# Optimization experiments

Measured on AMD Instinct MI355X. Metric: run time of the kernel, lower is better.

## Reference

```python
import jax, jax.numpy as jnp
import numpy as np


def setup_inputs() -> dict:
    key = jax.random.key(0)
    k1, k2 = jax.random.split(key)
    B, D, T = 8, 256, 4096
    Q, K = 8, 1024
    z = jax.random.normal(k1, (B, D, T), dtype=jnp.float32)
    # original init: uniform(-1/n_e, 1/n_e)
    codebooks = jax.random.uniform(k2, (Q, K, D), dtype=jnp.float32,
                                   minval=-1.0 / K, maxval=1.0 / K)
    return {"z": z, "codebooks": codebooks}


def reference(z, codebooks):
    # z: [B, e_dim, T]; codebooks: [Q, n_e, e_dim]
    zp = jnp.transpose(z, (0, 2, 1))  # [B, T, D]
    residual = zp
    quantized_out = jnp.zeros_like(zp)
    total_loss = jnp.zeros((), dtype=z.dtype)
    all_indices = []
    Q = codebooks.shape[0]
    for q in range(Q):  # small fixed number of residual stages
        E = codebooks[q]  # [K, D]
        # squared euclidean distances: ||r||^2 + ||e||^2 - 2 r.e
        d = (jnp.sum(residual ** 2, axis=-1, keepdims=True)
             + jnp.sum(E ** 2, axis=-1)
             - 2.0 * jnp.einsum('btd,kd->btk', residual, E))  # [B, T, K]
        idx = jnp.argmin(d, axis=-1)  # [B, T]
        z_q = E[idx]                  # [B, T, D] gather
        loss = (jnp.mean((jax.lax.stop_gradient(z_q) - residual) ** 2)
                + 0.25 * jnp.mean((z_q - jax.lax.stop_gradient(residual)) ** 2))
        # straight-through estimator
        z_q_st = residual + jax.lax.stop_gradient(z_q - residual)
        residual = residual - z_q_st
        quantized_out = quantized_out + z_q_st
        total_loss = total_loss + loss
        all_indices.append(idx)
    quantized_out = jnp.transpose(quantized_out, (0, 2, 1))  # [B, D, T]
    return quantized_out, total_loss, jnp.stack(all_indices)  # indices: [Q, B, T]
```

## Files before the change

kernel.cpp:

```cpp
#include <hip/hip_runtime.h>

#define B_   8
#define D_   256
#define T_   4096
#define Q_   8
#define K_   1024
#define BT_  (B_*T_)
#define N_   (B_*T_*D_)
#define LOSS_OFF N_
#define IDX_OFF  (N_+1)
#define ROWS 32

typedef __attribute__((ext_vector_type(8))) short short8;
typedef __attribute__((ext_vector_type(4))) float float4v;

union U4S8 { uint4 u; short8 s; };

__device__ __forceinline__ unsigned short f2bf(float x) {
    unsigned int u = __float_as_uint(x);
    unsigned int r = (u + 0x7FFFu + ((u >> 16) & 1u)) >> 16;
    return (unsigned short)r;
}
__device__ __forceinline__ float bf2f(unsigned short b) {
    return __uint_as_float(((unsigned int)b) << 16);
}
__device__ __forceinline__ unsigned fkey(float f) {
    unsigned u = __float_as_uint(f);
    return (u & 0x80000000u) ? ~u : (u | 0x80000000u);
}
__device__ __forceinline__ float fkeyinv(unsigned k) {
    unsigned u = (k & 0x80000000u) ? (k & 0x7fffffffu) : ~k;
    return __uint_as_float(u);
}


__global__ void k_init(const float* __restrict__ z, float* __restrict__ residual,
                       double* lossAcc, unsigned* MelU) {
    __shared__ float tile[32][33];
    int b  = blockIdx.z;
    int d0 = blockIdx.y * 32;
    int t0 = blockIdx.x * 32;
    int tx = threadIdx.x & 31;
    int ty = threadIdx.x >> 5;
    const float* zb = z + (size_t)b * D_ * T_;
    #pragma unroll
    for (int r = 0; r < 32; r += 8)
        tile[ty + r][tx] = zb[(size_t)(d0 + ty + r) * T_ + t0 + tx];
    __syncthreads();
    float* rb = residual + (size_t)b * T_ * D_;
    #pragma unroll
    for (int r = 0; r < 32; r += 8)
        rb[(size_t)(t0 + ty + r) * D_ + d0 + tx] = tile[tx][ty + r];
    if (b == 0 && blockIdx.x == 0 && blockIdx.y == 0 && threadIdx.x == 0) {
        *lossAcc = 0.0;
        #pragma unroll
        for (int i = 0; i < Q_; ++i) MelU[i] = 0u;
    }
}


__global__ void k_bfrag(const float* __restrict__ cb, uint4* __restrict__ Bfrag) {
    int gid = blockIdx.x * 256 + threadIdx.x;
    int q    = gid >> 15;
    int rem  = gid & 32767;
    int ct   = rem >> 9;
    int kc   = (rem >> 6) & 7;
    int lane = rem & 63;
    int cand = ct * 16 + (lane & 15);
    int kb   = kc * 32 + (lane >> 4) * 8;
    const float* e = cb + ((size_t)q * K_ + cand) * D_ + kb;
    float4v u0 = *(const float4v*)(e);
    float4v u1 = *(const float4v*)(e + 4);
    float vv[8] = {u0.x, u0.y, u0.z, u0.w, u1.x, u1.y, u1.z, u1.w};
    unsigned short h[8], l[8];
    #pragma unroll
    for (int j = 0; j < 8; ++j) {
        float v = vv[j];
        h[j] = f2bf(v);
        l[j] = f2bf(v - bf2f(h[j]));
    }
    uint4 hi, lo;
    hi.x = (unsigned)h[0] | ((unsigned)h[1] << 16);
    hi.y = (unsigned)h[2] | ((unsigned)h[3] << 16);
    hi.z = (unsigned)h[4] | ((unsigned)h[5] << 16);
    hi.w = (unsigned)h[6] | ((unsigned)h[7] << 16);
    lo.x = (unsigned)l[0] | ((unsigned)l[1] << 16);
    lo.y = (unsigned)l[2] | ((unsigned)l[3] << 16);
    lo.z = (unsigned)l[4] | ((unsigned)l[5] << 16);
    lo.w = (unsigned)l[6] | ((unsigned)l[7] << 16);
    size_t base = (((size_t)(q * 64 + ct) * 8 + kc) * 2) * 64;
    Bfrag[base + lane]      = hi;
    Bfrag[base + 64 + lane] = lo;
}


__global__ void k_se(const float* __restrict__ cb, float* __restrict__ Se,
                     unsigned* __restrict__ MelU) {
    int gid = blockIdx.x * 256 + threadIdx.x;
    int i  = gid >> 4;
    int ln = gid & 15;
    if (i >= Q_ * K_) return;
    const float* e = cb + (size_t)i * D_ + ln * 16;
    float4v v0 = *(const float4v*)(e);
    float4v v1 = *(const float4v*)(e + 4);
    float4v v2 = *(const float4v*)(e + 8);
    float4v v3 = *(const float4v*)(e + 12);
    float vv[16] = {v0.x, v0.y, v0.z, v0.w, v1.x, v1.y, v1.z, v1.w,
                    v2.x, v2.y, v2.z, v2.w, v3.x, v3.y, v3.z, v3.w};
    double s = 0.0, s2 = 0.0;
    #pragma unroll
    for (int d = 0; d < 16; ++d) {
        float v = vv[d];
        float a = v * v;
        s += (double)a;
        float el = v - bf2f(f2bf(v));
        s2 += (double)(el * el);
    }
    #pragma unroll
    for (int st = 8; st > 0; st >>= 1) {
        s  += __shfl_xor(s, st);
        s2 += __shfl_xor(s2, st);
    }
    if (ln == 0) {
        Se[i] = (float)s;
        atomicMax(&MelU[i >> 10], __float_as_uint((float)s2));
    }
}


__launch_bounds__(512, 2)
__global__ void k_stage(const float* __restrict__ cb,
                        const uint4* __restrict__ Bfrag,
                        const float* __restrict__ Se,
                        const float* __restrict__ Mel,
                        float* __restrict__ residual,
                        float* __restrict__ out,
                        double* __restrict__ lossAcc,
                        int q) {
    __shared__ union {
        uint4 afr[2048];
        struct { int slist[32][16]; float sdd[32][16];
                 int srow[512]; int sslot[512]; } post;
        struct { float ovd[512]; int ovk[512]; } over;
        double lred[8];
    } sc;
    __shared__ float seL[1024];
    __shared__ float srb[32], margin[32];
    __shared__ unsigned sminI[32];
    __shared__ int   scount[32], sidx[32];
    __shared__ int   nSurv;

    const int tid  = threadIdx.x;
    const int lane = tid & 63;
    const int w    = tid >> 6;
    const int quad = lane >> 4;
    const int lc   = lane & 15;
    const int row0 = blockIdx.x * ROWS;
    const int g    = tid >> 8;
    const int dt   = tid & 255;

    if (tid < 32) { scount[tid] = 0; sminI[tid] = 0xFFFFFFFFu; }
    if (tid == 32) nSurv = 0;
    seL[tid]       = Se[q * K_ + tid];
    seL[tid + 512] = Se[q * K_ + tid + 512];
    const float melq4 = 4.04f * sqrtf(Mel[q]);

    const uint4* __restrict__ Bq = Bfrag + (size_t)q * (64 * 8 * 2 * 64);
    U4S8 b0h, b1h;
    {
        const uint4* p0 = Bq + (((size_t)((w * 8 + 0) * 8 + 0)) * 2) * 64 + lane;
        b0h.u = p0[0];
        const uint4* p1 = Bq + (((size_t)((w * 8 + 1) * 8 + 0)) * 2) * 64 + lane;
        b1h.u = p1[0];
    }

    {
        int row = tid >> 4, seg = tid & 15;
        int rg = row >> 4, rlo = row & 15;
        int kc = seg >> 1, par = seg & 1;
        const float* rp = residual + (size_t)(row0 + row) * D_ + seg * 16;
        float4v v0 = *(const float4v*)(rp);
        float4v v1 = *(const float4v*)(rp + 4);
        float4v v2 = *(const float4v*)(rp + 8);
        float4v v3 = *(const float4v*)(rp + 12);
        float vv[16] = {v0.x, v0.y, v0.z, v0.w, v1.x, v1.y, v1.z, v1.w,
                        v2.x, v2.y, v2.z, v2.w, v3.x, v3.y, v3.z, v3.w};
        double s = 0.0; float sa = 0.0f;
        #pragma unroll
        for (int i = 0; i < 16; ++i) {
            float v = vv[i];
            s += (double)(v * v);
            sa += fabsf(v);
        }
        #pragma unroll
        for (int st = 8; st > 0; st >>= 1) {
            s  += __shfl_xor(s, st);
            sa += __shfl_xor(sa, st);
        }
        if (seg == 0) {
            float sr = (float)s;
            float sb = sa * 1.001f;
            srb[row]    = sr;
            margin[row] = 9.6e-7f * sr + 4.0e-7f * sb + 2.0e-4f
                        + melq4 * sqrtf(sr);
        }
        #pragma unroll
        for (int h = 0; h < 2; ++h) {
            unsigned short hh[8], ll[8];
            #pragma unroll
            for (int j = 0; j < 8; ++j) {
                float v = vv[h * 8 + j];
                hh[j] = f2bf(v);
                ll[j] = f2bf(v - bf2f(hh[j]));
            }
            uint4 hiW, loW;
            hiW.x = (unsigned)hh[0] | ((unsigned)hh[1] << 16);
            hiW.y = (unsigned)hh[2] | ((unsigned)hh[3] << 16);
            hiW.z = (unsigned)hh[4] | ((unsigned)hh[5] << 16);
            hiW.w = (unsigned)hh[6] | ((unsigned)hh[7] << 16);
            loW.x = (unsigned)ll[0] | ((unsigned)ll[1] << 16);
            loW.y = (unsigned)ll[2] | ((unsigned)ll[3] << 16);
            loW.z = (unsigned)ll[4] | ((unsigned)ll[5] << 16);
            loW.w = (unsigned)ll[6] | ((unsigned)ll[7] << 16);
            int ln = (par * 2 + h) * 16 + rlo;
            int sl = ln ^ kc;
            sc.afr[((rg * 8 + kc) * 2 + 0) * 64 + sl] = hiW;
            sc.afr[((rg * 8 + kc) * 2 + 1) * 64 + sl] = loW;
        }
    }
    __syncthreads();

    float4v accA[16];
    #pragma unroll
    for (int i = 0; i < 16; ++i) accA[i] = (float4v){0.f, 0.f, 0.f, 0.f};

    for (int kc = 0; kc < 8; ++kc) {
        U4S8 a0h, a0l, a1h, a1l;
        a0h.u = sc.afr[((0 * 8 + kc) * 2 + 0) * 64 + (lane ^ kc)];
        a0l.u = sc.afr[((0 * 8 + kc) * 2 + 1) * 64 + (lane ^ kc)];
        a1h.u = sc.afr[((1 * 8 + kc) * 2 + 0) * 64 + (lane ^ kc)];
        a1l.u = sc.afr[((1 * 8 + kc) * 2 + 1) * 64 + (lane ^ kc)];
        #pragma unroll
        for (int ctl = 0; ctl < 8; ++ctl) {
            U4S8 bh = ((ctl & 1) == 0) ? b0h : b1h;
            {
                int pkc  = kc + ((ctl + 2) >> 3);
                int pctl = (ctl + 2) & 7;
                const uint4* p = Bq + (((size_t)((w * 8 + pctl) * 8 + pkc)) * 2) * 64 + lane;
                if ((ctl & 1) == 0) b0h.u = p[0];
                else                b1h.u = p[0];
            }
            float4v a0 = accA[ctl * 2 + 0];
            a0 = __builtin_amdgcn_mfma_f32_16x16x32_bf16(a0h.s, bh.s, a0, 0, 0, 0);
            a0 = __builtin_amdgcn_mfma_f32_16x16x32_bf16(a0l.s, bh.s, a0, 0, 0, 0);
            accA[ctl * 2 + 0] = a0;
            float4v a1 = accA[ctl * 2 + 1];
            a1 = __builtin_amdgcn_mfma_f32_16x16x32_bf16(a1h.s, bh.s, a1, 0, 0, 0);
            a1 = __builtin_amdgcn_mfma_f32_16x16x32_bf16(a1l.s, bh.s, a1, 0, 0, 0);
            accA[ctl * 2 + 1] = a1;
        }
    }

    float sr8[8];
    #pragma unroll
    for (int rr = 0; rr < 8; ++rr)
        sr8[rr] = srb[(rr >> 2) * 16 + quad * 4 + (rr & 3)];

    float mn[8];
    #pragma unroll
    for (int rr = 0; rr < 8; ++rr) mn[rr] = 3.4e38f;
    #pragma unroll
    for (int ctl = 0; ctl < 8; ++ctl) {
        int cand = (w * 8 + ctl) * 16 + lc;
        float se = seL[cand];
        #pragma unroll
        for (int rr = 0; rr < 8; ++rr) {
            float dd = (sr8[rr] + se) - 2.0f * accA[ctl * 2 + (rr >> 2)][rr & 3];
            mn[rr] = fminf(mn[rr], dd);
        }
    }
    #pragma unroll
    for (int rr = 0; rr < 8; ++rr) {
        float v = mn[rr];
        v = fminf(v, __shfl_xor(v, 1));
        v = fminf(v, __shfl_xor(v, 2));
        v = fminf(v, __shfl_xor(v, 4));
        v = fminf(v, __shfl_xor(v, 8));
        if (lc == 0)
            atomicMin(&sminI[(rr >> 2) * 16 + quad * 4 + (rr & 3)], fkey(v));
    }
    __syncthreads();

    float thrV[8];
    #pragma unroll
    for (int rr = 0; rr < 8; ++rr) {
        int row = (rr >> 2) * 16 + quad * 4 + (rr & 3);
        thrV[rr] = fkeyinv(sminI[row]) + margin[row];
    }
    #pragma unroll
    for (int ctl = 0; ctl < 8; ++ctl) {
        int cand = (w * 8 + ctl) * 16 + lc;
        float se = seL[cand];
        #pragma unroll
        for (int rr = 0; rr < 8; ++rr) {
            int row = (rr >> 2) * 16 + quad * 4 + (rr & 3);
            float dd = (sr8[rr] + se) - 2.0f * accA[ctl * 2 + (rr >> 2)][rr & 3];
            if (dd <= thrV[rr]) {
                int p = atomicAdd(&scount[row], 1);
                if (p < 16) sc.post.slist[row][p] = cand;
            }
        }
    }
    __syncthreads();

    if (tid < 32) {
        int cnt = scount[tid];
        if (cnt == 1) {
            sidx[tid] = sc.post.slist[tid][0];
        } else if (cnt >= 2 && cnt <= 16) {
            int base = atomicAdd(&nSurv, cnt);
            for (int s2 = 0; s2 < cnt; ++s2) {
                sc.post.srow[base + s2]  = tid;
                sc.post.sslot[base + s2] = s2;
            }
        }
    }
    __syncthreads();

    {
        int nS  = nSurv;
        int grp = tid >> 4, ln = tid & 15;
        for (int j = grp; j < nS; j += 32) {
            int row  = sc.post.srow[j];
            int slot = sc.post.sslot[j];
            int k    = sc.post.slist[row][slot];
            const float* Ek = cb + ((size_t)q * K_ + k) * D_ + ln * 16;
            const float* Rk = residual + (size_t)(row0 + row) * D_ + ln * 16;
            float4v e0 = *(const float4v*)(Ek);
            float4v e1 = *(const float4v*)(Ek + 4);
            float4v e2 = *(const float4v*)(Ek + 8);
            float4v e3 = *(const float4v*)(Ek + 12);
            float4v r0 = *(const float4v*)(Rk);
            float4v r1 = *(const float4v*)(Rk + 4);
            float4v r2 = *(const float4v*)(Rk + 8);
            float4v r3 = *(const float4v*)(Rk + 12);
            float ev[16] = {e0.x, e0.y, e0.z, e0.w, e1.x, e1.y, e1.z, e1.w,
                            e2.x, e2.y, e2.z, e2.w, e3.x, e3.y, e3.z, e3.w};
            float rv2[16] = {r0.x, r0.y, r0.z, r0.w, r1.x, r1.y, r1.z, r1.w,
                             r2.x, r2.y, r2.z, r2.w, r3.x, r3.y, r3.z, r3.w};
            double a0 = 0.0, a1 = 0.0;
            #pragma unroll
            for (int d = 0; d < 16; d += 2) {
                a0 = fma((double)ev[d],     (double)rv2[d],     a0);
                a1 = fma((double)ev[d + 1], (double)rv2[d + 1], a1);
            }
            double ssum = a0 + a1;
            #pragma unroll
            for (int st = 8; st > 0; st >>= 1) ssum += __shfl_xor(ssum, st);
            if (ln == 0) {
                float dotf = (float)ssum;
                float V = srb[row] + seL[k];
                sc.post.sdd[row][slot] = V - 2.0f * dotf;
            }
        }
    }
    __syncthreads();
    if (tid < 32) {
        int cnt = scount[tid];
        if (cnt >= 2 && cnt <= 16) {
            float bd = 3.4e38f; int bk = 0x7fffffff;
            for (int s2 = 0; s2 < cnt; ++s2) {
                float dv = sc.post.sdd[tid][s2]; int kv = sc.post.slist[tid][s2];
                if (dv < bd || (dv == bd && kv < bk)) { bd = dv; bk = kv; }
            }
            sidx[tid] = bk;
        }
    }
    __syncthreads();

    for (int row = 0; row < ROWS; ++row) {
        int cnt = scount[row];
        if (cnt <= 16) continue;
        const float* Rr = residual + (size_t)(row0 + row) * D_;
        float bd = 3.4e38f; int bk = K_;
        #pragma unroll
        for (int c = 0; c < 2; ++c) {
            int k = tid * 2 + c;
            const float* Ek = cb + ((size_t)q * K_ + k) * D_;
            double a0 = 0.0, a1 = 0.0;
            for (int d = 0; d < D_; d += 2) {
                a0 = fma((double)Ek[d],     (double)Rr[d],     a0);
                a1 = fma((double)Ek[d + 1], (double)Rr[d + 1], a1);
            }
            float dd = (srb[row] + seL[k]) - 2.0f * (float)(a0 + a1);
            if (dd < bd || (dd == bd && k < bk)) { bd = dd; bk = k; }
        }
        sc.over.ovd[tid] = bd; sc.over.ovk[tid] = bk;
        __syncthreads();
        for (int st = 256; st > 0; st >>= 1) {
            if (tid < st) {
                float od = sc.over.ovd[tid + st]; int ok = sc.over.ovk[tid + st];
                if (od < sc.over.ovd[tid] ||
                    (od == sc.over.ovd[tid] && ok < sc.over.ovk[tid])) {
                    sc.over.ovd[tid] = od; sc.over.ovk[tid] = ok;
                }
            }
            __syncthreads();
        }
        if (tid == 0) sidx[row] = sc.over.ovk[0];
        __syncthreads();
    }

    const float* Eq = cb + (size_t)q * K_ * D_;
    double lsum = 0.0;
    #pragma unroll
    for (int jj = 0; jj < 16; ++jj) {
        int row = g * 16 + jj;
        int idx = sidx[row];
        size_t roff = (size_t)(row0 + row) * D_ + dt;
        float rv   = residual[roff];
        float zq   = Eq[(size_t)idx * D_ + dt];
        float t1   = zq - rv;
        float zqst = rv + t1;
        residual[roff] = rv - zqst;
        lsum += (double)t1 * (double)t1;
    }
    if (tid < 32) out[IDX_OFF + q * BT_ + row0 + tid] = (float)sidx[tid];

    #pragma unroll
    for (int st = 32; st > 0; st >>= 1) lsum += __shfl_xor(lsum, st);
    __syncthreads();
    if (lane == 0) sc.lred[w] = lsum;
    __syncthreads();
    if (tid == 0) {
        double t = 0.0;
        #pragma unroll
        for (int i = 0; i < 8; ++i) t += sc.lred[i];
        atomicAdd(lossAcc, t);
    }
}


__global__ void k_emit(const float* __restrict__ z, const float* __restrict__ residual,
                       float* __restrict__ out) {
    __shared__ float tile[32][33];
    int b  = blockIdx.z;
    int t0 = blockIdx.y * 32;
    int d0 = blockIdx.x * 32;
    int tx = threadIdx.x & 31;
    int ty = threadIdx.x >> 5;
    const float* rb = residual + (size_t)b * T_ * D_;
    #pragma unroll
    for (int r = 0; r < 32; r += 8)
        tile[ty + r][tx] = rb[(size_t)(t0 + ty + r) * D_ + d0 + tx];
    __syncthreads();
    const float* zb = z + (size_t)b * D_ * T_;
    float* ob = out + (size_t)b * D_ * T_;
    #pragma unroll
    for (int r = 0; r < 32; r += 8) {
        size_t off = (size_t)(d0 + ty + r) * T_ + t0 + tx;
        ob[off] = zb[off] - tile[tx][ty + r];
    }
}

__global__ void k_final(const double* lossAcc, float* out) {
    if (threadIdx.x == 0 && blockIdx.x == 0) {
        double m = *lossAcc / (double)N_;
        out[LOSS_OFF] = (float)(1.25 * m);
    }
}


extern "C" void kernel_launch(void* const* d_in, const int* in_sizes, int n_in,
                              void* d_out, int out_size, void* d_ws, size_t ws_size,
                              hipStream_t stream) {
    const float* z  = (const float*)d_in[0];
    const float* cb = (const float*)d_in[1];
    float* out = (float*)d_out;

    float*  residual = (float*)d_ws;
    uint4*  Bfrag    = (uint4*)((char*)d_ws + (size_t)N_ * 4);
    float*  Se       = (float*)((char*)d_ws + (size_t)N_ * 4 + (size_t)8 * 1024 * 1024);
    double* lossAcc  = (double*)((char*)d_ws + (size_t)N_ * 4 + (size_t)8 * 1024 * 1024
                                 + (size_t)Q_ * K_ * 4);
    unsigned* MelU   = (unsigned*)((char*)lossAcc + 8);

    hipLaunchKernelGGL(k_init, dim3(T_ / 32, D_ / 32, B_), dim3(256), 0, stream,
                       z, residual, lossAcc, MelU);
    hipLaunchKernelGGL(k_bfrag, dim3(1024), dim3(256), 0, stream, cb, Bfrag);
    hipLaunchKernelGGL(k_se, dim3((Q_ * K_ * 16 + 255) / 256), dim3(256), 0, stream,
                       cb, Se, MelU);
    for (int q = 0; q < Q_; ++q) {
        hipLaunchKernelGGL(k_stage, dim3(BT_ / ROWS), dim3(512), 0, stream,
                           cb, Bfrag, Se, (const float*)MelU, residual, out, lossAcc, q);
    }
    hipLaunchKernelGGL(k_emit, dim3(D_ / 32, T_ / 32, B_), dim3(256), 0, stream,
                       z, residual, out);
    hipLaunchKernelGGL(k_final, dim3(1), dim3(256), 0, stream, lossAcc, out);
}
```

Baseline: 915.6 us.

## Fuse pairs of residual quantization stages into one kernel with LDS-resident residual

Each launch now processes two consecutive codebook stages for the same 32 rows. The residual tile stays in a 32KB shared buffer between the two stages and is written to global memory only after the second stage. This halves the number of stage launches and removes one global read and write of the residual per pair. The extra shared memory may lower occupancy below the two blocks per CU the launch bounds request.

```diff
diff --git a/kernel.cpp b/kernel.cpp
--- a/kernel.cpp
+++ b/kernel.cpp
@@ -129,14 +129,15 @@
 
 
 __launch_bounds__(512, 2)
-__global__ void k_stage(const float* __restrict__ cb,
-                        const uint4* __restrict__ Bfrag,
-                        const float* __restrict__ Se,
-                        const float* __restrict__ Mel,
-                        float* __restrict__ residual,
-                        float* __restrict__ out,
-                        double* __restrict__ lossAcc,
-                        int q) {
+__global__ void k_stagepair(const float* __restrict__ cb,
+                            const uint4* __restrict__ Bfrag,
+                            const float* __restrict__ Se,
+                            const float* __restrict__ Mel,
+                            float* __restrict__ residual,
+                            float* __restrict__ out,
+                            double* __restrict__ lossAcc,
+                            int q0) {
+    __shared__ float rbuf[ROWS][256];
     __shared__ union {
         uint4 afr[2048];
         struct { int slist[32][16]; float sdd[32][16];
@@ -159,277 +160,298 @@
     const int g    = tid >> 8;
     const int dt   = tid & 255;
 
-    if (tid < 32) { scount[tid] = 0; sminI[tid] = 0xFFFFFFFFu; }
-    if (tid == 32) nSurv = 0;
-    seL[tid]       = Se[q * K_ + tid];
-    seL[tid + 512] = Se[q * K_ + tid + 512];
-    const float melq4 = 4.04f * sqrtf(Mel[q]);
-
-    const uint4* __restrict__ Bq = Bfrag + (size_t)q * (64 * 8 * 2 * 64);
-    U4S8 b0h, b1h;
-    {
-        const uint4* p0 = Bq + (((size_t)((w * 8 + 0) * 8 + 0)) * 2) * 64 + lane;
-        b0h.u = p0[0];
-        const uint4* p1 = Bq + (((size_t)((w * 8 + 1) * 8 + 0)) * 2) * 64 + lane;
-        b1h.u = p1[0];
-    }
-
-    {
-        int row = tid >> 4, seg = tid & 15;
-        int rg = row >> 4, rlo = row & 15;
-        int kc = seg >> 1, par = seg & 1;
-        const float* rp = residual + (size_t)(row0 + row) * D_ + seg * 16;
-        float4v v0 = *(const float4v*)(rp);
-        float4v v1 = *(const float4v*)(rp + 4);
-        float4v v2 = *(const float4v*)(rp + 8);
-        float4v v3 = *(const float4v*)(rp + 12);
-        float vv[16] = {v0.x, v0.y, v0.z, v0.w, v1.x, v1.y, v1.z, v1.w,
-                        v2.x, v2.y, v2.z, v2.w, v3.x, v3.y, v3.z, v3.w};
-        double s = 0.0; float sa = 0.0f;
-        #pragma unroll
-        for (int i = 0; i < 16; ++i) {
-            float v = vv[i];
-            s += (double)(v * v);
-            sa += fabsf(v);
-        }
-        #pragma unroll
-        for (int st = 8; st > 0; st >>= 1) {
-            s  += __shfl_xor(s, st);
-            sa += __shfl_xor(sa, st);
-        }
-        if (seg == 0) {
-            float sr = (float)s;
-            float sb = sa * 1.001f;
-            srb[row]    = sr;
-            margin[row] = 9.6e-7f * sr + 4.0e-7f * sb + 2.0e-4f
-                        + melq4 * sqrtf(sr);
-        }
-        #pragma unroll
-        for (int h = 0; h < 2; ++h) {
-            unsigned short hh[8], ll[8];
-            #pragma unroll
-            for (int j = 0; j < 8; ++j) {
-                float v = vv[h * 8 + j];
-                hh[j] = f2bf(v);
-                ll[j] = f2bf(v - bf2f(hh[j]));
-            }
-            uint4 hiW, loW;
-            hiW.x = (unsigned)hh[0] | ((unsigned)hh[1] << 16);
-            hiW.y = (unsigned)hh[2] | ((unsigned)hh[3] << 16);
-            hiW.z = (unsigned)hh[4] | ((unsigned)hh[5] << 16);
-            hiW.w = (unsigned)hh[6] | ((unsigned)hh[7] << 16);
-            loW.x = (unsigned)ll[0] | ((unsigned)ll[1] << 16);
-            loW.y = (unsigned)ll[2] | ((unsigned)ll[3] << 16);
-            loW.z = (unsigned)ll[4] | ((unsigned)ll[5] << 16);
-            loW.w = (unsigned)ll[6] | ((unsigned)ll[7] << 16);
-            int ln = (par * 2 + h) * 16 + rlo;
-            int sl = ln ^ kc;
-            sc.afr[((rg * 8 + kc) * 2 + 0) * 64 + sl] = hiW;
-            sc.afr[((rg * 8 + kc) * 2 + 1) * 64 + sl] = loW;
-        }
-    }
-    __syncthreads();
-
-    float4v accA[16];
-    #pragma unroll
-    for (int i = 0; i < 16; ++i) accA[i] = (float4v){0.f, 0.f, 0.f, 0.f};
-
-    for (int kc = 0; kc < 8; ++kc) {
-        U4S8 a0h, a0l, a1h, a1l;
-        a0h.u = sc.afr[((0 * 8 + kc) * 2 + 0) * 64 + (lane ^ kc)];
-        a0l.u = sc.afr[((0 * 8 + kc) * 2 + 1) * 64 + (lane ^ kc)];
-        a1h.u = sc.afr[((1 * 8 + kc) * 2 + 0) * 64 + (lane ^ kc)];
-        a1l.u = sc.afr[((1 * 8 + kc) * 2 + 1) * 64 + (lane ^ kc)];
+    double lsum = 0.0;
+
+    for (int qs = 0; qs < 2; ++qs) {
+        const int q = q0 + qs;
+
+        if (tid < 32) { scount[tid] = 0; sminI[tid] = 0xFFFFFFFFu; }
+        if (tid == 32) nSurv = 0;
+        seL[tid]       = Se[q * K_ + tid];
+        seL[tid + 512] = Se[q * K_ + tid + 512];
+        const float melq4 = 4.04f * sqrtf(Mel[q]);
+
+        const uint4* __restrict__ Bq = Bfrag + (size_t)q * (64 * 8 * 2 * 64);
+        U4S8 b0h, b1h;
+        {
+            const uint4* p0 = Bq + (((size_t)((w * 8 + 0) * 8 + 0)) * 2) * 64 + lane;
+            b0h.u = p0[0];
+            const uint4* p1 = Bq + (((size_t)((w * 8 + 1) * 8 + 0)) * 2) * 64 + lane;
+            b1h.u = p1[0];
+        }
+
+        {
+            int row = tid >> 4, seg = tid & 15;
+            int rg = row >> 4, rlo = row & 15;
+            int kc = seg >> 1, par = seg & 1;
+            float4v v0, v1, v2, v3;
+            if (qs == 0) {
+                const float* rp = residual + (size_t)(row0 + row) * D_ + seg * 16;
+                v0 = *(const float4v*)(rp);
+                v1 = *(const float4v*)(rp + 4);
+                v2 = *(const float4v*)(rp + 8);
+                v3 = *(const float4v*)(rp + 12);
+                float* lp = &rbuf[row][seg * 16];
+                *(float4v*)(lp)      = v0;
+                *(float4v*)(lp + 4)  = v1;
+                *(float4v*)(lp + 8)  = v2;
+                *(float4v*)(lp + 12) = v3;
+            } else {
+                const float* lp = &rbuf[row][seg * 16];
+                v0 = *(const float4v*)(lp);
+                v1 = *(const float4v*)(lp + 4);
+                v2 = *(const float4v*)(lp + 8);
+                v3 = *(const float4v*)(lp + 12);
+            }
+            float vv[16] = {v0.x, v0.y, v0.z, v0.w, v1.x, v1.y, v1.z, v1.w,
+                            v2.x, v2.y, v2.z, v2.w, v3.x, v3.y, v3.z, v3.w};
+            double s = 0.0; float sa = 0.0f;
+            #pragma unroll
+            for (int i = 0; i < 16; ++i) {
+                float v = vv[i];
+                s += (double)(v * v);
+                sa += fabsf(v);
+            }
+            #pragma unroll
+            for (int st = 8; st > 0; st >>= 1) {
+                s  += __shfl_xor(s, st);
+                sa += __shfl_xor(sa, st);
+            }
+            if (seg == 0) {
+                float sr = (float)s;
+                float sb = sa * 1.001f;
+                srb[row]    = sr;
+                margin[row] = 9.6e-7f * sr + 4.0e-7f * sb + 2.0e-4f
+                            + melq4 * sqrtf(sr);
+            }
+            #pragma unroll
+            for (int h = 0; h < 2; ++h) {
+                unsigned short hh[8], ll[8];
+                #pragma unroll
+                for (int j = 0; j < 8; ++j) {
+                    float v = vv[h * 8 + j];
+                    hh[j] = f2bf(v);
+                    ll[j] = f2bf(v - bf2f(hh[j]));
+                }
+                uint4 hiW, loW;
+                hiW.x = (unsigned)hh[0] | ((unsigned)hh[1] << 16);
+                hiW.y = (unsigned)hh[2] | ((unsigned)hh[3] << 16);
+                hiW.z = (unsigned)hh[4] | ((unsigned)hh[5] << 16);
+                hiW.w = (unsigned)hh[6] | ((unsigned)hh[7] << 16);
+                loW.x = (unsigned)ll[0] | ((unsigned)ll[1] << 16);
+                loW.y = (unsigned)ll[2] | ((unsigned)ll[3] << 16);
+                loW.z = (unsigned)ll[4] | ((unsigned)ll[5] << 16);
+                loW.w = (unsigned)ll[6] | ((unsigned)ll[7] << 16);
+                int ln = (par * 2 + h) * 16 + rlo;
+                int sl = ln ^ kc;
+                sc.afr[((rg * 8 + kc) * 2 + 0) * 64 + sl] = hiW;
+                sc.afr[((rg * 8 + kc) * 2 + 1) * 64 + sl] = loW;
+            }
+        }
+        __syncthreads();
+
+        float4v accA[16];
+        #pragma unroll
+        for (int i = 0; i < 16; ++i) accA[i] = (float4v){0.f, 0.f, 0.f, 0.f};
+
+        for (int kc = 0; kc < 8; ++kc) {
+            U4S8 a0h, a0l, a1h, a1l;
+            a0h.u = sc.afr[((0 * 8 + kc) * 2 + 0) * 64 + (lane ^ kc)];
+            a0l.u = sc.afr[((0 * 8 + kc) * 2 + 1) * 64 + (lane ^ kc)];
+            a1h.u = sc.afr[((1 * 8 + kc) * 2 + 0) * 64 + (lane ^ kc)];
+            a1l.u = sc.afr[((1 * 8 + kc) * 2 + 1) * 64 + (lane ^ kc)];
+            #pragma unroll
+            for (int ctl = 0; ctl < 8; ++ctl) {
+                U4S8 bh = ((ctl & 1) == 0) ? b0h : b1h;
+                {
+                    int pkc  = kc + ((ctl + 2) >> 3);
+                    int pctl = (ctl + 2) & 7;
+                    const uint4* p = Bq + (((size_t)((w * 8 + pctl) * 8 + pkc)) * 2) * 64 + lane;
+                    if ((ctl & 1) == 0) b0h.u = p[0];
+                    else                b1h.u = p[0];
+                }
+                float4v a0 = accA[ctl * 2 + 0];
+                a0 = __builtin_amdgcn_mfma_f32_16x16x32_bf16(a0h.s, bh.s, a0, 0, 0, 0);
+                a0 = __builtin_amdgcn_mfma_f32_16x16x32_bf16(a0l.s, bh.s, a0, 0, 0, 0);
+                accA[ctl * 2 + 0] = a0;
+                float4v a1 = accA[ctl * 2 + 1];
+                a1 = __builtin_amdgcn_mfma_f32_16x16x32_bf16(a1h.s, bh.s, a1, 0, 0, 0);
+                a1 = __builtin_amdgcn_mfma_f32_16x16x32_bf16(a1l.s, bh.s, a1, 0, 0, 0);
+                accA[ctl * 2 + 1] = a1;
+            }
+        }
+
+        float sr8[8];
+        #pragma unroll
+        for (int rr = 0; rr < 8; ++rr)
+            sr8[rr] = srb[(rr >> 2) * 16 + quad * 4 + (rr & 3)];
+
+        float mn[8];
+        #pragma unroll
+        for (int rr = 0; rr < 8; ++rr) mn[rr] = 3.4e38f;
         #pragma unroll
         for (int ctl = 0; ctl < 8; ++ctl) {
-            U4S8 bh = ((ctl & 1) == 0) ? b0h : b1h;
-            {
-                int pkc  = kc + ((ctl + 2) >> 3);
-                int pctl = (ctl + 2) & 7;
-                const uint4* p = Bq + (((size_t)((w * 8 + pctl) * 8 + pkc)) * 2) * 64 + lane;
-                if ((ctl & 1) == 0) b0h.u = p[0];
-                else                b1h.u = p[0];
-            }
-            float4v a0 = accA[ctl * 2 + 0];
-            a0 = __builtin_amdgcn_mfma_f32_16x16x32_bf16(a0h.s, bh.s, a0, 0, 0, 0);
-            a0 = __builtin_amdgcn_mfma_f32_16x16x32_bf16(a0l.s, bh.s, a0, 0, 0, 0);
-            accA[ctl * 2 + 0] = a0;
-            float4v a1 = accA[ctl * 2 + 1];
-            a1 = __builtin_amdgcn_mfma_f32_16x16x32_bf16(a1h.s, bh.s, a1, 0, 0, 0);
-            a1 = __builtin_amdgcn_mfma_f32_16x16x32_bf16(a1l.s, bh.s, a1, 0, 0, 0);
-            accA[ctl * 2 + 1] = a1;
-        }
-    }
-
-    float sr8[8];
-    #pragma unroll
-    for (int rr = 0; rr < 8; ++rr)
-        sr8[rr] = srb[(rr >> 2) * 16 + quad * 4 + (rr & 3)];
-
-    float mn[8];
-    #pragma unroll
-    for (int rr = 0; rr < 8; ++rr) mn[rr] = 3.4e38f;
-    #pragma unroll
-    for (int ctl = 0; ctl < 8; ++ctl) {
-        int cand = (w * 8 + ctl) * 16 + lc;
-        float se = seL[cand];
+            int cand = (w * 8 + ctl) * 16 + lc;
+            float se = seL[cand];
+            #pragma unroll
+            for (int rr = 0; rr < 8; ++rr) {
+                float dd = (sr8[rr] + se) - 2.0f * accA[ctl * 2 + (rr >> 2)][rr & 3];
+                mn[rr] = fminf(mn[rr], dd);
+            }
+        }
         #pragma unroll
         for (int rr = 0; rr < 8; ++rr) {
-            float dd = (sr8[rr] + se) - 2.0f * accA[ctl * 2 + (rr >> 2)][rr & 3];
-            mn[rr] = fminf(mn[rr], dd);
-        }
-    }
-    #pragma unroll
-    for (int rr = 0; rr < 8; ++rr) {
-        float v = mn[rr];
-        v = fminf(v, __shfl_xor(v, 1));
-        v = fminf(v, __shfl_xor(v, 2));
-        v = fminf(v, __shfl_xor(v, 4));
-        v = fminf(v, __shfl_xor(v, 8));
-        if (lc == 0)
-            atomicMin(&sminI[(rr >> 2) * 16 + quad * 4 + (rr & 3)], fkey(v));
-    }
-    __syncthreads();
-
-    float thrV[8];
-    #pragma unroll
-    for (int rr = 0; rr < 8; ++rr) {
-        int row = (rr >> 2) * 16 + quad * 4 + (rr & 3);
-        thrV[rr] = fkeyinv(sminI[row]) + margin[row];
-    }
-    #pragma unroll
-    for (int ctl = 0; ctl < 8; ++ctl) {
-        int cand = (w * 8 + ctl) * 16 + lc;
-        float se = seL[cand];
+            float v = mn[rr];
+            v = fminf(v, __shfl_xor(v, 1));
+            v = fminf(v, __shfl_xor(v, 2));
+            v = fminf(v, __shfl_xor(v, 4));
+            v = fminf(v, __shfl_xor(v, 8));
+            if (lc == 0)
+                atomicMin(&sminI[(rr >> 2) * 16 + quad * 4 + (rr & 3)], fkey(v));
+        }
+        __syncthreads();
+
+        float thrV[8];
         #pragma unroll
         for (int rr = 0; rr < 8; ++rr) {
             int row = (rr >> 2) * 16 + quad * 4 + (rr & 3);
-            float dd = (sr8[rr] + se) - 2.0f * accA[ctl * 2 + (rr >> 2)][rr & 3];
-            if (dd <= thrV[rr]) {
-                int p = atomicAdd(&scount[row], 1);
-                if (p < 16) sc.post.slist[row][p] = cand;
-            }
-        }
-    }
-    __syncthreads();
-
-    if (tid < 32) {
-        int cnt = scount[tid];
-        if (cnt == 1) {
-            sidx[tid] = sc.post.slist[tid][0];
-        } else if (cnt >= 2 && cnt <= 16) {
-            int base = atomicAdd(&nSurv, cnt);
-            for (int s2 = 0; s2 < cnt; ++s2) {
-                sc.post.srow[base + s2]  = tid;
-                sc.post.sslot[base + s2] = s2;
-            }
-        }
-    }
-    __syncthreads();
-
-    {
-        int nS  = nSurv;
-        int grp = tid >> 4, ln = tid & 15;
-        for (int j = grp; j < nS; j += 32) {
-            int row  = sc.post.srow[j];
-            int slot = sc.post.sslot[j];
-            int k    = sc.post.slist[row][slot];
-            const float* Ek = cb + ((size_t)q * K_ + k) * D_ + ln * 16;
-            const float* Rk = residual + (size_t)(row0 + row) * D_ + ln * 16;
-            float4v e0 = *(const float4v*)(Ek);
-            float4v e1 = *(const float4v*)(Ek + 4);
-            float4v e2 = *(const float4v*)(Ek + 8);
-            float4v e3 = *(const float4v*)(Ek + 12);
-            float4v r0 = *(const float4v*)(Rk);
-            float4v r1 = *(const float4v*)(Rk + 4);
-            float4v r2 = *(const float4v*)(Rk + 8);
-            float4v r3 = *(const float4v*)(Rk + 12);
-            float ev[16] = {e0.x, e0.y, e0.z, e0.w, e1.x, e1.y, e1.z, e1.w,
-                            e2.x, e2.y, e2.z, e2.w, e3.x, e3.y, e3.z, e3.w};
-            float rv2[16] = {r0.x, r0.y, r0.z, r0.w, r1.x, r1.y, r1.z, r1.w,
-                             r2.x, r2.y, r2.z, r2.w, r3.x, r3.y, r3.z, r3.w};
-            double a0 = 0.0, a1 = 0.0;
-            #pragma unroll
-            for (int d = 0; d < 16; d += 2) {
-                a0 = fma((double)ev[d],     (double)rv2[d],     a0);
-                a1 = fma((double)ev[d + 1], (double)rv2[d + 1], a1);
-            }
-            double ssum = a0 + a1;
-            #pragma unroll
-            for (int st = 8; st > 0; st >>= 1) ssum += __shfl_xor(ssum, st);
-            if (ln == 0) {
-                float dotf = (float)ssum;
-                float V = srb[row] + seL[k];
-                sc.post.sdd[row][slot] = V - 2.0f * dotf;
-            }
-        }
-    }
-    __syncthreads();
-    if (tid < 32) {
-        int cnt = scount[tid];
-        if (cnt >= 2 && cnt <= 16) {
-            float bd = 3.4e38f; int bk = 0x7fffffff;
-            for (int s2 = 0; s2 < cnt; ++s2) {
-                float dv = sc.post.sdd[tid][s2]; int kv = sc.post.slist[tid][s2];
-                if (dv < bd || (dv == bd && kv < bk)) { bd = dv; bk = kv; }
-            }
-            sidx[tid] = bk;
-        }
-    }
-    __syncthreads();
-
-    for (int row = 0; row < ROWS; ++row) {
-        int cnt = scount[row];
-        if (cnt <= 16) continue;
-        const float* Rr = residual + (size_t)(row0 + row) * D_;
-        float bd = 3.4e38f; int bk = K_;
-        #pragma unroll
-        for (int c = 0; c < 2; ++c) {
-            int k = tid * 2 + c;
-            const float* Ek = cb + ((size_t)q * K_ + k) * D_;
-            double a0 = 0.0, a1 = 0.0;
-            for (int d = 0; d < D_; d += 2) {
-                a0 = fma((double)Ek[d],     (double)Rr[d],     a0);
-                a1 = fma((double)Ek[d + 1], (double)Rr[d + 1], a1);
-            }
-            float dd = (srb[row] + seL[k]) - 2.0f * (float)(a0 + a1);
-            if (dd < bd || (dd == bd && k < bk)) { bd = dd; bk = k; }
-        }
-        sc.over.ovd[tid] = bd; sc.over.ovk[tid] = bk;
-        __syncthreads();
-        for (int st = 256; st > 0; st >>= 1) {
-            if (tid < st) {
-                float od = sc.over.ovd[tid + st]; int ok = sc.over.ovk[tid + st];
-                if (od < sc.over.ovd[tid] ||
-                    (od == sc.over.ovd[tid] && ok < sc.over.ovk[tid])) {
-                    sc.over.ovd[tid] = od; sc.over.ovk[tid] = ok;
-                }
-            }
+            thrV[rr] = fkeyinv(sminI[row]) + margin[row];
+        }
+        #pragma unroll
+        for (int ctl = 0; ctl < 8; ++ctl) {
+            int cand = (w * 8 + ctl) * 16 + lc;
+            float se = seL[cand];
+            #pragma unroll
+            for (int rr = 0; rr < 8; ++rr) {
+                int row = (rr >> 2) * 16 + quad * 4 + (rr & 3);
+                float dd = (sr8[rr] + se) - 2.0f * accA[ctl * 2 + (rr >> 2)][rr & 3];
+                if (dd <= thrV[rr]) {
+                    int p = atomicAdd(&scount[row], 1);
+                    if (p < 16) sc.post.slist[row][p] = cand;
+                }
+            }
+        }
+        __syncthreads();
+
+        if (tid < 32) {
+            int cnt = scount[tid];
+            if (cnt == 1) {
+                sidx[tid] = sc.post.slist[tid][0];
+            } else if (cnt >= 2 && cnt <= 16) {
+                int base = atomicAdd(&nSurv, cnt);
+                for (int s2 = 0; s2 < cnt; ++s2) {
+                    sc.post.srow[base + s2]  = tid;
+                    sc.post.sslot[base + s2] = s2;
+                }
+            }
+        }
+        __syncthreads();
+
+        {
+            int nS  = nSurv;
+            int grp = tid >> 4, ln = tid & 15;
+            for (int j = grp; j < nS; j += 32) {
+                int row  = sc.post.srow[j];
+                int slot = sc.post.sslot[j];
+                int k    = sc.post.slist[row][slot];
+                const float* Ek = cb + ((size_t)q * K_ + k) * D_ + ln * 16;
+                const float* Rk = &rbuf[row][ln * 16];
+                float4v e0 = *(const float4v*)(Ek);
+                float4v e1 = *(const float4v*)(Ek + 4);
+                float4v e2 = *(const float4v*)(Ek + 8);
+                float4v e3 = *(const float4v*)(Ek + 12);
+                float4v r0 = *(const float4v*)(Rk);
+                float4v r1 = *(const float4v*)(Rk + 4);
+                float4v r2 = *(const float4v*)(Rk + 8);
+                float4v r3 = *(const float4v*)(Rk + 12);
+                float ev[16] = {e0.x, e0.y, e0.z, e0.w, e1.x, e1.y, e1.z, e1.w,
+                                e2.x, e2.y, e2.z, e2.w, e3.x, e3.y, e3.z, e3.w};
+                float rv2[16] = {r0.x, r0.y, r0.z, r0.w, r1.x, r1.y, r1.z, r1.w,
+                                 r2.x, r2.y, r2.z, r2.w, r3.x, r3.y, r3.z, r3.w};
+                double a0 = 0.0, a1 = 0.0;
+                #pragma unroll
+                for (int d = 0; d < 16; d += 2) {
+                    a0 = fma((double)ev[d],     (double)rv2[d],     a0);
+                    a1 = fma((double)ev[d + 1], (double)rv2[d + 1], a1);
+                }
+                double ssum = a0 + a1;
+                #pragma unroll
+                for (int st = 8; st > 0; st >>= 1) ssum += __shfl_xor(ssum, st);
+                if (ln == 0) {
+                    float dotf = (float)ssum;
+                    float V = srb[row] + seL[k];
+                    sc.post.sdd[row][slot] = V - 2.0f * dotf;
+                }
+            }
+        }
+        __syncthreads();
+        if (tid < 32) {
+            int cnt = scount[tid];
+            if (cnt >= 2 && cnt <= 16) {
+                float bd = 3.4e38f; int bk = 0x7fffffff;
+                for (int s2 = 0; s2 < cnt; ++s2) {
+                    float dv = sc.post.sdd[tid][s2]; int kv = sc.post.slist[tid][s2];
+                    if (dv < bd || (dv == bd && kv < bk)) { bd = dv; bk = kv; }
+                }
+                sidx[tid] = bk;
+            }
+        }
+        __syncthreads();
+
+        for (int row = 0; row < ROWS; ++row) {
+            int cnt = scount[row];
+            if (cnt <= 16) continue;
+            float bd = 3.4e38f; int bk = K_;
+            #pragma unroll
+            for (int c = 0; c < 2; ++c) {
+                int k = tid * 2 + c;
+                const float* Ek = cb + ((size_t)q * K_ + k) * D_;
+                double a0 = 0.0, a1 = 0.0;
+                for (int d = 0; d < D_; d += 2) {
+                    a0 = fma((double)Ek[d],     (double)rbuf[row][d],     a0);
+                    a1 = fma((double)Ek[d + 1], (double)rbuf[row][d + 1], a1);
+                }
+                float dd = (srb[row] + seL[k]) - 2.0f * (float)(a0 + a1);
+                if (dd < bd || (dd == bd && k < bk)) { bd = dd; bk = k; }
+            }
+            sc.over.ovd[tid] = bd; sc.over.ovk[tid] = bk;
             __syncthreads();
-        }
-        if (tid == 0) sidx[row] = sc.over.ovk[0];
-        __syncthreads();
-    }
-
-    const float* Eq = cb + (size_t)q * K_ * D_;
-    double lsum = 0.0;
-    #pragma unroll
-    for (int jj = 0; jj < 16; ++jj) {
-        int row = g * 16 + jj;
-        int idx = sidx[row];
-        size_t roff = (size_t)(row0 + row) * D_ + dt;
-        float rv   = residual[roff];
-        float zq   = Eq[(size_t)idx * D_ + dt];
-        float t1   = zq - rv;
-        float zqst = rv + t1;
-        residual[roff] = rv - zqst;
-        lsum += (double)t1 * (double)t1;
-    }
-    if (tid < 32) out[IDX_OFF + q * BT_ + row0 + tid] = (float)sidx[tid];
+            for (int st = 256; st > 0; st >>= 1) {
+                if (tid < st) {
+                    float od = sc.over.ovd[tid + st]; int ok = sc.over.ovk[tid + st];
+                    if (od < sc.over.ovd[tid] ||
+                        (od == sc.over.ovd[tid] && ok < sc.over.ovk[tid])) {
+                        sc.over.ovd[tid] = od; sc.over.ovk[tid] = ok;
+                    }
+                }
+                __syncthreads();
+            }
+            if (tid == 0) sidx[row] = sc.over.ovk[0];
+            __syncthreads();
+        }
+
+        const float* Eq = cb + (size_t)q * K_ * D_;
+        #pragma unroll
+        for (int jj = 0; jj < 16; ++jj) {
+            int row = g * 16 + jj;
+            int idx = sidx[row];
+            float rv   = rbuf[row][dt];
+            float zq   = Eq[(size_t)idx * D_ + dt];
+            float t1   = zq - rv;
+            float zqst = rv + t1;
+            float nr   = rv - zqst;
+            rbuf[row][dt] = nr;
+            if (qs == 1)
+                residual[(size_t)(row0 + row) * D_ + dt] = nr;
+            lsum += (double)t1 * (double)t1;
+        }
+        if (tid < 32) out[IDX_OFF + q * BT_ + row0 + tid] = (float)sidx[tid];
+
+        __syncthreads();
+    }
 
     #pragma unroll
     for (int st = 32; st > 0; st >>= 1) lsum += __shfl_xor(lsum, st);
-    __syncthreads();
     if (lane == 0) sc.lred[w] = lsum;
     __syncthreads();
     if (tid == 0) {
@@ -490,9 +512,9 @@
     hipLaunchKernelGGL(k_bfrag, dim3(1024), dim3(256), 0, stream, cb, Bfrag);
     hipLaunchKernelGGL(k_se, dim3((Q_ * K_ * 16 + 255) / 256), dim3(256), 0, stream,
                        cb, Se, MelU);
-    for (int q = 0; q < Q_; ++q) {
-        hipLaunchKernelGGL(k_stage, dim3(BT_ / ROWS), dim3(512), 0, stream,
-                           cb, Bfrag, Se, (const float*)MelU, residual, out, lossAcc, q);
+    for (int q0 = 0; q0 < Q_; q0 += 2) {
+        hipLaunchKernelGGL(k_stagepair, dim3(BT_ / ROWS), dim3(512), 0, stream,
+                           cb, Bfrag, Se, (const float*)MelU, residual, out, lossAcc, q0);
     }
     hipLaunchKernelGGL(k_emit, dim3(D_ / 32, T_ / 32, B_), dim3(256), 0, stream,
                        z, residual, out);
```

Result: slower. 1.114 ms (+21.7%).
